# Kernel optimization log

Hardware: AMD Instinct MI355X
Metric: run time of the kernel (lower is better)

The kernel has to match this reference:

```python
import jax, jax.numpy as jnp
import numpy as np

NUM_LAYERS = 2
H = 8        # num_head
D = 64       # dim_head
HID = H * D  # hidden_size = 512
FF = 2048    # dim_ff
SLEN = 256
BSZ = 16
IN_DIM = 512


def setup_inputs() -> dict:
    key = jax.random.key(0)
    ks = jax.random.split(key, 12)
    std = 1.0 / np.sqrt(D)
    return {
        'x': jax.random.normal(ks[0], (SLEN, BSZ, IN_DIM), jnp.float32),
        'in_w': jax.random.normal(ks[1], (IN_DIM, HID), jnp.float32) * 0.02,
        'in_b': jnp.zeros((HID,), jnp.float32),
        'Wy': jax.random.normal(ks[2], (NUM_LAYERS, H, D, D), jnp.float32) * std,
        'Wq': jax.random.normal(ks[3], (NUM_LAYERS, H, D, D), jnp.float32) * std,
        'Wk': jax.random.normal(ks[4], (NUM_LAYERS, H, D, D), jnp.float32) * std,
        'wb': jax.random.normal(ks[5], (NUM_LAYERS, H, D, 4), jnp.float32) * std,
        'Wout': jax.random.normal(ks[6], (NUM_LAYERS, HID, HID), jnp.float32) * 0.02,
        'ln_g': jnp.ones((NUM_LAYERS, HID), jnp.float32),
        'ln_b': jnp.zeros((NUM_LAYERS, HID), jnp.float32),
        'ff_w1': jax.random.normal(ks[7], (NUM_LAYERS, HID, FF), jnp.float32) * 0.02,
        'ff_b1': jnp.zeros((NUM_LAYERS, FF), jnp.float32),
        'ff_w2': jax.random.normal(ks[8], (NUM_LAYERS, FF, HID), jnp.float32) * 0.02,
        'ff_b2': jnp.zeros((NUM_LAYERS, HID), jnp.float32),
        'core_state': 0,
    }


def _layer_norm(x, g, b):
    m = jnp.mean(x, axis=-1, keepdims=True)
    v = jnp.mean(jnp.square(x - m), axis=-1, keepdims=True)
    return (x - m) / jnp.sqrt(v + 1e-5) * g + b


def _sr_block(h, Wy0, Wq0, Wk0, wb0, Wout_l):
    # h: [L, B, HID]. Self-referential fast-weight recurrence (self_ref_v0).
    L, B, _ = h.shape
    x = jax.nn.softmax(h.reshape(L, B, H, D), axis=-1)  # [L,B,H,D]
    init = (
        jnp.broadcast_to(Wy0, (B, H, D, D)),
        jnp.broadcast_to(Wq0, (B, H, D, D)),
        jnp.broadcast_to(Wk0, (B, H, D, D)),
        jnp.broadcast_to(wb0, (B, H, D, 4)),
    )

    def step(carry, xt):
        Wy_, Wq_, Wk_, wb_ = carry
        y = jnp.einsum('bhij,bhj->bhi', Wy_, xt)
        q = jax.nn.softmax(jnp.einsum('bhij,bhj->bhi', Wq_, xt), axis=-1)
        k = jax.nn.softmax(jnp.einsum('bhij,bhj->bhi', Wk_, xt), axis=-1)
        beta = jax.nn.sigmoid(jnp.einsum('bhjf,bhj->bhf', wb_, xt))  # [B,H,4]
        d = q - k
        dy = jnp.einsum('bhij,bhj->bhi', Wy_, d)  # W(q) - W(k) by linearity
        dq = jnp.einsum('bhij,bhj->bhi', Wq_, d)
        dk = jnp.einsum('bhij,bhj->bhi', Wk_, d)
        db = jnp.einsum('bhjf,bhj->bhf', wb_, d)  # [B,H,4]
        kT = k[..., None, :]  # [B,H,1,D]
        Wy_n = Wy_ + beta[..., 0:1, None] * dy[..., :, None] * kT
        Wq_n = Wq_ + beta[..., 1:2, None] * dq[..., :, None] * kT
        Wk_n = Wk_ + beta[..., 2:3, None] * dk[..., :, None] * kT
        wb_n = wb_ + beta[..., 3][..., None, None] * k[..., :, None] * db[..., None, :]
        return (Wy_n, Wq_n, Wk_n, wb_n), y

    _, ys = jax.lax.scan(step, init, x)            # ys: [L,B,H,D]
    out = ys.reshape(L, B, H * D) @ Wout_l          # out_linear (no bias)
    return h + out


def reference(x, in_w, in_b, Wy, Wq, Wk, wb, Wout, ln_g, ln_b,
              ff_w1, ff_b1, ff_w2, ff_b2, core_state):
    out = x @ in_w + in_b  # input_proj
    for i in range(NUM_LAYERS):
        out = _sr_block(out, Wy[i], Wq[i], Wk[i], wb[i], Wout[i])
        y = _layer_norm(out, ln_g[i], ln_b[i])
        out = out + (jax.nn.relu(y @ ff_w1[i] + ff_b1[i]) @ ff_w2[i] + ff_b2[i])
    return out
```

## Files before the change

### kernel.cpp

```cpp
#include <hip/hip_runtime.h>
#include <hip/hip_bf16.h>
#include <math.h>

#define SLEN 256
#define BSZ  16
#define NH   8
#define HD   64
#define HID  512
#define FFD  2048
#define MROWS (SLEN*BSZ)

typedef __attribute__((ext_vector_type(8))) short short8v;
typedef __attribute__((ext_vector_type(4))) float float4v;
typedef unsigned short ushort_t;

#define SYNC_LDS() do { \
  asm volatile("s_waitcnt lgkmcnt(0)" ::: "memory"); \
  __builtin_amdgcn_s_barrier(); \
} while (0)

template<int C> __device__ __forceinline__ float dppf(float x){
  return __int_as_float(__builtin_amdgcn_update_dpp(__float_as_int(x), __float_as_int(x), C, 0xF, 0xF, false));
}

__device__ __forceinline__ float rsum64(float v){
  v += dppf<0xB1>(v);
  v += dppf<0x4E>(v);
  v += dppf<0x141>(v);
  v += dppf<0x140>(v);
  v += __int_as_float(__builtin_amdgcn_update_dpp(0, __float_as_int(v), 0x142, 0xa, 0xF, false));
  v += __int_as_float(__builtin_amdgcn_update_dpp(0, __float_as_int(v), 0x143, 0xc, 0xF, false));
  return __int_as_float(__builtin_amdgcn_readlane(__float_as_int(v), 63));
}

__device__ __forceinline__ void split_bf16(float f, ushort_t& h, ushort_t& l){
  unsigned u = __float_as_uint(f);
  unsigned r = u + (0x7fffu + ((u >> 16) & 1u));
  h = (ushort_t)(r >> 16);
  float hf = __uint_as_float(((unsigned)h) << 16);
  float lo = f - hf;
  unsigned u2 = __float_as_uint(lo);
  unsigned r2 = u2 + (0x7fffu + ((u2 >> 16) & 1u));
  l = (ushort_t)(r2 >> 16);
}

template<int N, int K, bool BIAS, bool RESID, bool RELU>
__global__ __launch_bounds__(512) void gemm_mfma(
    const float* __restrict__ A, const float* __restrict__ B,
    const float* __restrict__ bias, const float* __restrict__ resid,
    float* __restrict__ C)
{
  __shared__ ushort_t Ah[128][40];
  __shared__ ushort_t Al[128][40];
  __shared__ ushort_t Bh[128][40];
  __shared__ ushort_t Bl[128][40];

  const int tid = threadIdx.x;
  const int wv = tid >> 6, lane = tid & 63;
  const int wm = wv >> 2, wn = wv & 3;
  const int l15 = lane & 15, l16 = lane >> 4;
  const int row0 = blockIdx.y * 128, col0 = blockIdx.x * 128;

  const int sar = tid >> 2, sak = (tid & 3) * 8;
  const int sbc = tid & 127, sbk = (tid >> 7) * 8;

  float4v acc[4][2];
#pragma unroll
  for (int i = 0; i < 4; ++i)
#pragma unroll
    for (int n = 0; n < 2; ++n) acc[i][n] = (float4v)(0.f);

  for (int k0 = 0; k0 < K; k0 += 32) {
    {
      const float* ap = &A[(size_t)(row0 + sar) * K + k0 + sak];
      float4 a0 = *reinterpret_cast<const float4*>(ap);
      float4 a1 = *reinterpret_cast<const float4*>(ap + 4);
      float av[8] = {a0.x, a0.y, a0.z, a0.w, a1.x, a1.y, a1.z, a1.w};
      short8v vh, vl;
#pragma unroll
      for (int j = 0; j < 8; ++j) {
        ushort_t h, l; split_bf16(av[j], h, l);
        vh[j] = (short)h; vl[j] = (short)l;
      }
      *reinterpret_cast<short8v*>(&Ah[sar][sak]) = vh;
      *reinterpret_cast<short8v*>(&Al[sar][sak]) = vl;
    }
    {
      float bv[8];
#pragma unroll
      for (int j = 0; j < 8; ++j)
        bv[j] = B[(size_t)(k0 + sbk + j) * N + col0 + sbc];
      short8v vh, vl;
#pragma unroll
      for (int j = 0; j < 8; ++j) {
        ushort_t h, l; split_bf16(bv[j], h, l);
        vh[j] = (short)h; vl[j] = (short)l;
      }
      *reinterpret_cast<short8v*>(&Bh[sbc][sbk]) = vh;
      *reinterpret_cast<short8v*>(&Bl[sbc][sbk]) = vl;
    }
    __syncthreads();

    short8v ah[4], al[4], bh[2], bl[2];
#pragma unroll
    for (int i = 0; i < 4; ++i) {
      const int r = wm * 64 + i * 16 + l15;
      ah[i] = *reinterpret_cast<const short8v*>(&Ah[r][l16 * 8]);
      al[i] = *reinterpret_cast<const short8v*>(&Al[r][l16 * 8]);
    }
#pragma unroll
    for (int n = 0; n < 2; ++n) {
      const int c = wn * 32 + n * 16 + l15;
      bh[n] = *reinterpret_cast<const short8v*>(&Bh[c][l16 * 8]);
      bl[n] = *reinterpret_cast<const short8v*>(&Bl[c][l16 * 8]);
    }
#pragma unroll
    for (int i = 0; i < 4; ++i)
#pragma unroll
      for (int n = 0; n < 2; ++n) {
        acc[i][n] = __builtin_amdgcn_mfma_f32_16x16x32_bf16(ah[i], bh[n], acc[i][n], 0, 0, 0);
        acc[i][n] = __builtin_amdgcn_mfma_f32_16x16x32_bf16(ah[i], bl[n], acc[i][n], 0, 0, 0);
        acc[i][n] = __builtin_amdgcn_mfma_f32_16x16x32_bf16(al[i], bh[n], acc[i][n], 0, 0, 0);
      }
    __syncthreads();
  }

#pragma unroll
  for (int i = 0; i < 4; ++i) {
#pragma unroll
    for (int n = 0; n < 2; ++n) {
      const int col = col0 + wn * 32 + n * 16 + l15;
      float bs = BIAS ? bias[col] : 0.f;
#pragma unroll
      for (int r = 0; r < 4; ++r) {
        const int row = row0 + wm * 64 + i * 16 + l16 * 4 + r;
        float v = acc[i][n][r] + bs;
        if (RESID) v += resid[(size_t)row * N + col];
        if (RELU)  v = fmaxf(v, 0.f);
        C[(size_t)row * N + col] = v;
      }
    }
  }
}

__global__ __launch_bounds__(64) void layernorm_k(
    const float* __restrict__ in, const float* __restrict__ g,
    const float* __restrict__ b, float* __restrict__ out)
{
  const int row = blockIdx.x, lane = threadIdx.x;
  const float* p = in + (size_t)row * HID + lane * 8;
  float4 v0 = *reinterpret_cast<const float4*>(p);
  float4 v1 = *reinterpret_cast<const float4*>(p + 4);
  float s = v0.x + v0.y + v0.z + v0.w + v1.x + v1.y + v1.z + v1.w;
  s = rsum64(s);
  const float mean = s * (1.0f / HID);
  float x[8] = {v0.x, v0.y, v0.z, v0.w, v1.x, v1.y, v1.z, v1.w};
  float sq = 0.f;
#pragma unroll
  for (int j = 0; j < 8; ++j) { float d = x[j] - mean; sq += d * d; }
  sq = rsum64(sq);
  const float rstd = rsqrtf(sq * (1.0f / HID) + 1e-5f);
  float4 g0 = *reinterpret_cast<const float4*>(&g[lane * 8]);
  float4 g1 = *reinterpret_cast<const float4*>(&g[lane * 8 + 4]);
  float4 b0 = *reinterpret_cast<const float4*>(&b[lane * 8]);
  float4 b1 = *reinterpret_cast<const float4*>(&b[lane * 8 + 4]);
  float gg[8] = {g0.x, g0.y, g0.z, g0.w, g1.x, g1.y, g1.z, g1.w};
  float bb[8] = {b0.x, b0.y, b0.z, b0.w, b1.x, b1.y, b1.z, b1.w};
  float o[8];
#pragma unroll
  for (int j = 0; j < 8; ++j) o[j] = (x[j] - mean) * rstd * gg[j] + bb[j];
  float4 o0 = make_float4(o[0], o[1], o[2], o[3]);
  float4 o1 = make_float4(o[4], o[5], o[6], o[7]);
  float* q = out + (size_t)row * HID + lane * 8;
  *reinterpret_cast<float4*>(q) = o0;
  *reinterpret_cast<float4*>(q + 4) = o1;
}

__global__ __launch_bounds__(256) void srec4t(
    const float* __restrict__ h,
    const float* __restrict__ Wy0, const float* __restrict__ Wq0,
    const float* __restrict__ Wk0, const float* __restrict__ wb0,
    float* __restrict__ ys)
{
  const int bh = blockIdx.x;
  const int bb = bh >> 3, hh = bh & 7;
  const int tid = threadIdx.x;
  const int wv = tid >> 6, lane = tid & 63;

  __shared__ float xs[2][64];
  __shared__ float q_s[2][64];
  __shared__ float k_s[2][64];
  __shared__ float4 betas4[2];

  float W[64];
  float wbr[4] = {0.f, 0.f, 0.f, 0.f};
  float xrA = 0.f, xrB = 0.f;
  float xnreg = 0.f;

  const float* xp = h + (size_t)bb * HID + hh * 64 + lane;
  float* yp = ys + (size_t)bb * HID + hh * 64 + lane;

  if (wv < 3) {
    const float* base = (wv == 0 ? Wy0 : (wv == 1 ? Wq0 : Wk0)) + (size_t)(hh * 64 + lane) * 64;
#pragma unroll
    for (int j = 0; j < 16; ++j) {
      float4 a = reinterpret_cast<const float4*>(base)[j];
      W[4*j] = a.x; W[4*j+1] = a.y; W[4*j+2] = a.z; W[4*j+3] = a.w;
    }
  } else {
    float4 w = *reinterpret_cast<const float4*>(&wb0[(size_t)(hh * 64 + lane) * 4]);
    wbr[0] = w.x; wbr[1] = w.y; wbr[2] = w.z; wbr[3] = w.w;
    float xr0 = xp[0];
    xrA = xp[(size_t)BSZ * HID];
    float e = __expf(xr0);
    float sm = rsum64(e);
    float x0 = e * __builtin_amdgcn_rcpf(sm);
    xs[0][lane] = x0;
    float s0 = rsum64(wbr[0] * x0);
    float s1 = rsum64(wbr[1] * x0);
    float s2 = rsum64(wbr[2] * x0);
    float s3 = rsum64(wbr[3] * x0);
    if (lane == 0)
      betas4[0] = make_float4(__builtin_amdgcn_rcpf(1.f + __expf(-s0)),
                              __builtin_amdgcn_rcpf(1.f + __expf(-s1)),
                              __builtin_amdgcn_rcpf(1.f + __expf(-s2)),
                              __builtin_amdgcn_rcpf(1.f + __expf(-s3)));
  }
  SYNC_LDS();

  auto stepf = [&](int P, float& XCUR, float& XNEXT, int T) {
    if (wv == 3) {
      if (T + 2 < SLEN) XNEXT = xp[(size_t)(T + 2) * BSZ * HID];
      float e = __expf(XCUR);
      float sm = rsum64(e);
      float xn_ = e * __builtin_amdgcn_rcpf(sm);
      xs[1 - P][lane] = xn_;
      xnreg = xn_;
    } else {
      const float4* xv = reinterpret_cast<const float4*>(xs[P]);
      float a0=0.f,a1=0.f,a2=0.f,a3=0.f,a4=0.f,a5=0.f,a6=0.f,a7=0.f;
#pragma unroll
      for (int j = 0; j < 8; ++j) {
        float4 x1 = xv[2*j], x2 = xv[2*j+1];
        a0 = fmaf(W[8*j+0], x1.x, a0);
        a1 = fmaf(W[8*j+1], x1.y, a1);
        a2 = fmaf(W[8*j+2], x1.z, a2);
        a3 = fmaf(W[8*j+3], x1.w, a3);
        a4 = fmaf(W[8*j+4], x2.x, a4);
        a5 = fmaf(W[8*j+5], x2.y, a5);
        a6 = fmaf(W[8*j+6], x2.z, a6);
        a7 = fmaf(W[8*j+7], x2.w, a7);
      }
      float acc = ((a0 + a1) + (a2 + a3)) + ((a4 + a5) + (a6 + a7));
      if (wv == 0) {
        yp[(size_t)T * BSZ * HID] = acc;
      } else {
        float e = __expf(acc);
        float sm = rsum64(e);
        float v = e * __builtin_amdgcn_rcpf(sm);
        float* dst = (wv == 1) ? q_s[P] : k_s[P];
        dst[lane] = v;
      }
    }

    SYNC_LDS();

    float4 bb4 = betas4[P];
    if (wv < 3) {
      const float4* qv = reinterpret_cast<const float4*>(q_s[P]);
      const float4* kv = reinterpret_cast<const float4*>(k_s[P]);
      float4 karr[16];
      float a0=0.f,a1=0.f,a2=0.f,a3=0.f,a4=0.f,a5=0.f,a6=0.f,a7=0.f;
#pragma unroll
      for (int j = 0; j < 8; ++j) {
        float4 q1 = qv[2*j], k1 = kv[2*j];
        float4 q2 = qv[2*j+1], k2 = kv[2*j+1];
        karr[2*j] = k1; karr[2*j+1] = k2;
        a0 = fmaf(W[8*j+0], q1.x - k1.x, a0);
        a1 = fmaf(W[8*j+1], q1.y - k1.y, a1);
        a2 = fmaf(W[8*j+2], q1.z - k1.z, a2);
        a3 = fmaf(W[8*j+3], q1.w - k1.w, a3);
        a4 = fmaf(W[8*j+4], q2.x - k2.x, a4);
        a5 = fmaf(W[8*j+5], q2.y - k2.y, a5);
        a6 = fmaf(W[8*j+6], q2.z - k2.z, a6);
        a7 = fmaf(W[8*j+7], q2.w - k2.w, a7);
      }
      float dd = ((a0 + a1) + (a2 + a3)) + ((a4 + a5) + (a6 + a7));
      float beta = (wv == 0) ? bb4.x : (wv == 1 ? bb4.y : bb4.z);
      float c = beta * dd;
#pragma unroll
      for (int j = 0; j < 16; ++j) {
        float4 k4 = karr[j];
        W[4*j]   = fmaf(c, k4.x, W[4*j]);
        W[4*j+1] = fmaf(c, k4.y, W[4*j+1]);
        W[4*j+2] = fmaf(c, k4.z, W[4*j+2]);
        W[4*j+3] = fmaf(c, k4.w, W[4*j+3]);
      }
    } else {
      float ql = q_s[P][lane], kl = k_s[P][lane];
      float dl = ql - kl;
      float bk = bb4.w * kl;
      float u0 = rsum64(wbr[0] * xnreg);
      float u1 = rsum64(wbr[1] * xnreg);
      float u2 = rsum64(wbr[2] * xnreg);
      float u3 = rsum64(wbr[3] * xnreg);
      float d0 = rsum64(wbr[0] * dl);
      float d1 = rsum64(wbr[1] * dl);
      float d2 = rsum64(wbr[2] * dl);
      float d3 = rsum64(wbr[3] * dl);
      float g  = rsum64(bk * xnreg);
      wbr[0] = fmaf(bk, d0, wbr[0]);
      wbr[1] = fmaf(bk, d1, wbr[1]);
      wbr[2] = fmaf(bk, d2, wbr[2]);
      wbr[3] = fmaf(bk, d3, wbr[3]);
      float s0 = fmaf(d0, g, u0);
      float s1 = fmaf(d1, g, u1);
      float s2 = fmaf(d2, g, u2);
      float s3 = fmaf(d3, g, u3);
      if (lane == 0)
        betas4[1 - P] = make_float4(__builtin_amdgcn_rcpf(1.f + __expf(-s0)),
                                    __builtin_amdgcn_rcpf(1.f + __expf(-s1)),
                                    __builtin_amdgcn_rcpf(1.f + __expf(-s2)),
                                    __builtin_amdgcn_rcpf(1.f + __expf(-s3)));
    }
  };

  for (int t = 0; t < SLEN; t += 2) {
    stepf(0, xrA, xrB, t);
    stepf(1, xrB, xrA, t + 1);
  }
}

extern "C" void kernel_launch(void* const* d_in, const int* in_sizes, int n_in,
                              void* d_out, int out_size, void* d_ws, size_t ws_size,
                              hipStream_t stream)
{
  const float* x     = (const float*)d_in[0];
  const float* in_w  = (const float*)d_in[1];
  const float* in_b  = (const float*)d_in[2];
  const float* Wy    = (const float*)d_in[3];
  const float* Wq    = (const float*)d_in[4];
  const float* Wk    = (const float*)d_in[5];
  const float* wb    = (const float*)d_in[6];
  const float* Wout  = (const float*)d_in[7];
  const float* ln_g  = (const float*)d_in[8];
  const float* ln_b  = (const float*)d_in[9];
  const float* ff_w1 = (const float*)d_in[10];
  const float* ff_b1 = (const float*)d_in[11];
  const float* ff_w2 = (const float*)d_in[12];
  const float* ff_b2 = (const float*)d_in[13];
  float* out = (float*)d_out;

  char* ws = (char*)d_ws;
  float* ys   = (float*)ws;
  float* ffb  = (float*)(ws + (8u << 20));
  float* ybuf = (float*)(ws + (40u << 20));

  gemm_mfma<HID, 512, true, false, false><<<dim3(HID/128, MROWS/128), 512, 0, stream>>>(
      x, in_w, in_b, nullptr, out);

  for (int l = 0; l < 2; ++l) {
    srec4t<<<128, 256, 0, stream>>>(out,
                                    Wy + (size_t)l * NH * HD * HD,
                                    Wq + (size_t)l * NH * HD * HD,
                                    Wk + (size_t)l * NH * HD * HD,
                                    wb + (size_t)l * NH * HD * 4,
                                    ys);
    gemm_mfma<HID, HID, false, true, false><<<dim3(HID/128, MROWS/128), 512, 0, stream>>>(
        ys, Wout + (size_t)l * HID * HID, nullptr, out, out);
    layernorm_k<<<MROWS, 64, 0, stream>>>(out, ln_g + (size_t)l * HID, ln_b + (size_t)l * HID, ybuf);
    gemm_mfma<FFD, HID, true, false, true><<<dim3(FFD/128, MROWS/128), 512, 0, stream>>>(
        ybuf, ff_w1 + (size_t)l * HID * FFD, ff_b1 + (size_t)l * FFD, nullptr, ffb);
    gemm_mfma<HID, FFD, true, true, false><<<dim3(HID/128, MROWS/128), 512, 0, stream>>>(
        ffb, ff_w2 + (size_t)l * FFD * HID, ff_b2 + (size_t)l * HID, out, out);
  }
}
```

Measured before the change: 943.9 us.

## Pre-split and transpose weights to bf16 hi/lo; producers emit packed bf16 pairs

Adds a split_wT kernel that transposes each weight matrix once per call and splits it into bf16 hi/lo halves. The GEMMs can then load B tiles as contiguous vectors instead of strided scalar loads, with no per-tile conversion. Producers (the fast-weight kernel, layernorm, FF1) now write activations as packed hi/lo uint32 pairs, so consuming GEMMs skip the split arithmetic. The trade is extra weight preprocessing launches each call and more workspace, with the same numerics as before.

```diff
diff --git a/kernel.cpp b/kernel.cpp
--- a/kernel.cpp
+++ b/kernel.cpp
@@ -13,6 +13,7 @@
 typedef __attribute__((ext_vector_type(8))) short short8v;
 typedef __attribute__((ext_vector_type(4))) float float4v;
 typedef unsigned short ushort_t;
+typedef unsigned int uint_t;
 
 #define SYNC_LDS() do { \
   asm volatile("s_waitcnt lgkmcnt(0)" ::: "memory"); \
@@ -44,11 +45,28 @@
   l = (ushort_t)(r2 >> 16);
 }
 
-template<int N, int K, bool BIAS, bool RESID, bool RELU>
-__global__ __launch_bounds__(512) void gemm_mfma(
-    const float* __restrict__ A, const float* __restrict__ B,
+__device__ __forceinline__ uint_t pack_bf16(float f){
+  ushort_t h, l; split_bf16(f, h, l);
+  return ((uint_t)h << 16) | (uint_t)l;
+}
+
+__global__ __launch_bounds__(256) void split_wT(
+    const float* __restrict__ W, ushort_t* __restrict__ Th, ushort_t* __restrict__ Tl,
+    int Kd, int Nd)
+{
+  int idx = blockIdx.x * 256 + threadIdx.x;
+  int n = idx / Kd, k = idx - n * Kd;
+  float v = W[(size_t)k * Nd + n];
+  ushort_t h, l; split_bf16(v, h, l);
+  Th[idx] = h; Tl[idx] = l;
+}
+
+template<int N, int K, int AMODE, bool BIAS, bool RESID, bool RELU, bool PACKOUT>
+__global__ __launch_bounds__(512) void gemm_bt(
+    const void* __restrict__ Ax,
+    const ushort_t* __restrict__ BhT, const ushort_t* __restrict__ BlT,
     const float* __restrict__ bias, const float* __restrict__ resid,
-    float* __restrict__ C)
+    void* __restrict__ Cx)
 {
   __shared__ ushort_t Ah[128][40];
   __shared__ ushort_t Al[128][40];
@@ -72,32 +90,35 @@
 
   for (int k0 = 0; k0 < K; k0 += 32) {
     {
-      const float* ap = &A[(size_t)(row0 + sar) * K + k0 + sak];
-      float4 a0 = *reinterpret_cast<const float4*>(ap);
-      float4 a1 = *reinterpret_cast<const float4*>(ap + 4);
-      float av[8] = {a0.x, a0.y, a0.z, a0.w, a1.x, a1.y, a1.z, a1.w};
       short8v vh, vl;
-#pragma unroll
-      for (int j = 0; j < 8; ++j) {
-        ushort_t h, l; split_bf16(av[j], h, l);
-        vh[j] = (short)h; vl[j] = (short)l;
+      if (AMODE == 0) {
+        const float* ap = (const float*)Ax + (size_t)(row0 + sar) * K + k0 + sak;
+        float4 a0 = *reinterpret_cast<const float4*>(ap);
+        float4 a1 = *reinterpret_cast<const float4*>(ap + 4);
+        float av[8] = {a0.x, a0.y, a0.z, a0.w, a1.x, a1.y, a1.z, a1.w};
+#pragma unroll
+        for (int j = 0; j < 8; ++j) {
+          ushort_t h, l; split_bf16(av[j], h, l);
+          vh[j] = (short)h; vl[j] = (short)l;
+        }
+      } else {
+        const uint_t* ap = (const uint_t*)Ax + (size_t)(row0 + sar) * K + k0 + sak;
+        uint4 a0 = *reinterpret_cast<const uint4*>(ap);
+        uint4 a1 = *reinterpret_cast<const uint4*>(ap + 4);
+        uint_t av[8] = {a0.x, a0.y, a0.z, a0.w, a1.x, a1.y, a1.z, a1.w};
+#pragma unroll
+        for (int j = 0; j < 8; ++j) {
+          vh[j] = (short)(av[j] >> 16);
+          vl[j] = (short)(av[j] & 0xffffu);
+        }
       }
       *reinterpret_cast<short8v*>(&Ah[sar][sak]) = vh;
       *reinterpret_cast<short8v*>(&Al[sar][sak]) = vl;
     }
     {
-      float bv[8];
-#pragma unroll
-      for (int j = 0; j < 8; ++j)
-        bv[j] = B[(size_t)(k0 + sbk + j) * N + col0 + sbc];
-      short8v vh, vl;
-#pragma unroll
-      for (int j = 0; j < 8; ++j) {
-        ushort_t h, l; split_bf16(bv[j], h, l);
-        vh[j] = (short)h; vl[j] = (short)l;
-      }
-      *reinterpret_cast<short8v*>(&Bh[sbc][sbk]) = vh;
-      *reinterpret_cast<short8v*>(&Bl[sbc][sbk]) = vl;
+      const size_t bo = (size_t)(col0 + sbc) * K + k0 + sbk;
+      *reinterpret_cast<short8v*>(&Bh[sbc][sbk]) = *reinterpret_cast<const short8v*>(BhT + bo);
+      *reinterpret_cast<short8v*>(&Bl[sbc][sbk]) = *reinterpret_cast<const short8v*>(BlT + bo);
     }
     __syncthreads();
 
@@ -137,7 +158,8 @@
         float v = acc[i][n][r] + bs;
         if (RESID) v += resid[(size_t)row * N + col];
         if (RELU)  v = fmaxf(v, 0.f);
-        C[(size_t)row * N + col] = v;
+        if (PACKOUT) ((uint_t*)Cx)[(size_t)row * N + col] = pack_bf16(v);
+        else         ((float*)Cx)[(size_t)row * N + col] = v;
       }
     }
   }
@@ -145,7 +167,7 @@
 
 __global__ __launch_bounds__(64) void layernorm_k(
     const float* __restrict__ in, const float* __restrict__ g,
-    const float* __restrict__ b, float* __restrict__ out)
+    const float* __restrict__ b, uint_t* __restrict__ out)
 {
   const int row = blockIdx.x, lane = threadIdx.x;
   const float* p = in + (size_t)row * HID + lane * 8;
@@ -166,21 +188,21 @@
   float4 b1 = *reinterpret_cast<const float4*>(&b[lane * 8 + 4]);
   float gg[8] = {g0.x, g0.y, g0.z, g0.w, g1.x, g1.y, g1.z, g1.w};
   float bb[8] = {b0.x, b0.y, b0.z, b0.w, b1.x, b1.y, b1.z, b1.w};
-  float o[8];
-#pragma unroll
-  for (int j = 0; j < 8; ++j) o[j] = (x[j] - mean) * rstd * gg[j] + bb[j];
-  float4 o0 = make_float4(o[0], o[1], o[2], o[3]);
-  float4 o1 = make_float4(o[4], o[5], o[6], o[7]);
-  float* q = out + (size_t)row * HID + lane * 8;
-  *reinterpret_cast<float4*>(q) = o0;
-  *reinterpret_cast<float4*>(q + 4) = o1;
+  uint_t o[8];
+#pragma unroll
+  for (int j = 0; j < 8; ++j) o[j] = pack_bf16((x[j] - mean) * rstd * gg[j] + bb[j]);
+  uint4 o0 = make_uint4(o[0], o[1], o[2], o[3]);
+  uint4 o1 = make_uint4(o[4], o[5], o[6], o[7]);
+  uint_t* q = out + (size_t)row * HID + lane * 8;
+  *reinterpret_cast<uint4*>(q) = o0;
+  *reinterpret_cast<uint4*>(q + 4) = o1;
 }
 
 __global__ __launch_bounds__(256) void srec4t(
     const float* __restrict__ h,
     const float* __restrict__ Wy0, const float* __restrict__ Wq0,
     const float* __restrict__ Wk0, const float* __restrict__ wb0,
-    float* __restrict__ ys)
+    uint_t* __restrict__ ys)
 {
   const int bh = blockIdx.x;
   const int bb = bh >> 3, hh = bh & 7;
@@ -198,7 +220,7 @@
   float xnreg = 0.f;
 
   const float* xp = h + (size_t)bb * HID + hh * 64 + lane;
-  float* yp = ys + (size_t)bb * HID + hh * 64 + lane;
+  uint_t* yp = ys + (size_t)bb * HID + hh * 64 + lane;
 
   if (wv < 3) {
     const float* base = (wv == 0 ? Wy0 : (wv == 1 ? Wq0 : Wk0)) + (size_t)(hh * 64 + lane) * 64;
@@ -253,7 +275,7 @@
       }
       float acc = ((a0 + a1) + (a2 + a3)) + ((a4 + a5) + (a6 + a7));
       if (wv == 0) {
-        yp[(size_t)T * BSZ * HID] = acc;
+        yp[(size_t)T * BSZ * HID] = pack_bf16(acc);
       } else {
         float e = __expf(acc);
         float sm = rsum64(e);
@@ -352,12 +374,26 @@
   float* out = (float*)d_out;
 
   char* ws = (char*)d_ws;
-  float* ys   = (float*)ws;
-  float* ffb  = (float*)(ws + (8u << 20));
-  float* ybuf = (float*)(ws + (40u << 20));
-
-  gemm_mfma<HID, 512, true, false, false><<<dim3(HID/128, MROWS/128), 512, 0, stream>>>(
-      x, in_w, in_b, nullptr, out);
+  uint_t* ys   = (uint_t*)ws;
+  uint_t* ffb  = (uint_t*)(ws + (8u  << 20));
+  uint_t* ybuf = (uint_t*)(ws + (40u << 20));
+  char*   wsp  = ws + (48u << 20);
+
+  ushort_t* in_wT_h = (ushort_t*)wsp;
+  ushort_t* in_wT_l = (ushort_t*)(wsp + (512u << 10));
+  auto lw = [&](int l, int off_kb) -> ushort_t* {
+    return (ushort_t*)(wsp + (1024u << 10) + (size_t)l * (9216u << 10) + ((size_t)off_kb << 10));
+  };
+
+  split_wT<<<(512*512)/256, 256, 0, stream>>>(in_w, in_wT_h, in_wT_l, 512, HID);
+  for (int l = 0; l < 2; ++l) {
+    split_wT<<<(HID*HID)/256, 256, 0, stream>>>(Wout + (size_t)l*HID*HID, lw(l,0),    lw(l,512),  HID, HID);
+    split_wT<<<(HID*FFD)/256, 256, 0, stream>>>(ff_w1 + (size_t)l*HID*FFD, lw(l,1024), lw(l,3072), HID, FFD);
+    split_wT<<<(FFD*HID)/256, 256, 0, stream>>>(ff_w2 + (size_t)l*FFD*HID, lw(l,5120), lw(l,7168), FFD, HID);
+  }
+
+  gemm_bt<HID, 512, 0, true, false, false, false><<<dim3(HID/128, MROWS/128), 512, 0, stream>>>(
+      x, in_wT_h, in_wT_l, in_b, nullptr, out);
 
   for (int l = 0; l < 2; ++l) {
     srec4t<<<128, 256, 0, stream>>>(out,
@@ -366,12 +402,12 @@
                                     Wk + (size_t)l * NH * HD * HD,
                                     wb + (size_t)l * NH * HD * 4,
                                     ys);
-    gemm_mfma<HID, HID, false, true, false><<<dim3(HID/128, MROWS/128), 512, 0, stream>>>(
-        ys, Wout + (size_t)l * HID * HID, nullptr, out, out);
+    gemm_bt<HID, HID, 1, false, true, false, false><<<dim3(HID/128, MROWS/128), 512, 0, stream>>>(
+        ys, lw(l,0), lw(l,512), nullptr, out, out);
     layernorm_k<<<MROWS, 64, 0, stream>>>(out, ln_g + (size_t)l * HID, ln_b + (size_t)l * HID, ybuf);
-    gemm_mfma<FFD, HID, true, false, true><<<dim3(FFD/128, MROWS/128), 512, 0, stream>>>(
-        ybuf, ff_w1 + (size_t)l * HID * FFD, ff_b1 + (size_t)l * FFD, nullptr, ffb);
-    gemm_mfma<HID, FFD, true, true, false><<<dim3(HID/128, MROWS/128), 512, 0, stream>>>(
-        ffb, ff_w2 + (size_t)l * FFD * HID, ff_b2 + (size_t)l * HID, out, out);
-  }
-}
+    gemm_bt<FFD, HID, 1, true, false, true, true><<<dim3(FFD/128, MROWS/128), 512, 0, stream>>>(
+        ybuf, lw(l,1024), lw(l,3072), ff_b1 + (size_t)l * FFD, nullptr, ffb);
+    gemm_bt<HID, FFD, 1, true, true, false, false><<<dim3(HID/128, MROWS/128), 512, 0, stream>>>(
+        ffb, lw(l,5120), lw(l,7168), ff_b2 + (size_t)l * HID, out, out);
+  }
+}
```

New measurement: 1.071 ms. +13.4%, slower.
